# Kernel optimization log

Hardware: AMD Instinct MI355X
Metric: run time of the kernel (lower is better)

Reference implementation:

```python
import jax, jax.numpy as jnp
import numpy as np
from jax import lax

H = 16          # attention heads
N_LAYERS = 2    # encoder applies the SAME (shared-weight) layer N times
FILTERS = (1, 3, 5)
EPS_LN = 1e-6
EPS_BN = 1e-5


def _ln(x, a, b):
    # torch LayerNorm variant: unbiased std, eps added to std (not var)
    m = x.mean(-1, keepdims=True)
    s = jnp.std(x, axis=-1, keepdims=True, ddof=1)
    return a * (x - m) / (s + EPS_LN) + b


def _mha(x, wq, bq, wk, bk, wv, bv, wo, bo):
    B, S, D = x.shape
    dk = D // H
    def proj(w, b):
        return (x @ w + b).reshape(B, S, H, dk).transpose(0, 2, 1, 3)  # bhsd
    q, k, v = proj(wq, bq), proj(wk, bk), proj(wv, bv)
    scores = jnp.einsum('bhqd,bhkd->bhqk', q, k) / jnp.sqrt(jnp.float32(dk))
    p = jax.nn.softmax(scores, axis=-1)  # dropout is identity in eval mode
    o = jnp.einsum('bhqk,bhkd->bhqd', p, v)
    o = o.transpose(0, 2, 1, 3).reshape(B, S, D)
    return o @ wo + bo


def _conv_branch(xt, w, b, g, beta, m, v):
    # xt: [B, C, L]; w: [out, in, f]; BatchNorm1d in eval mode (running stats)
    f = w.shape[-1]
    y = lax.conv_general_dilated(xt, w, window_strides=(1,),
                                 padding=[(f // 2, f // 2)],
                                 dimension_numbers=('NCH', 'OIH', 'NCH'))
    y = y + b[None, :, None]
    y = (y - m[None, :, None]) / jnp.sqrt(v[None, :, None] + EPS_BN)
    y = y * g[None, :, None] + beta[None, :, None]
    return jax.nn.relu(y)


def setup_inputs() -> dict:
    key = jax.random.key(0)
    B, S, D = 8, 1024, 1024
    ks = iter(jax.random.split(key, 64))
    nrm = lambda shape, sc=0.02: jax.random.normal(next(ks), shape, jnp.float32) * sc
    inp = {'x': jax.random.normal(next(ks), (B, S, D), jnp.float32)}
    for nm in ('wq', 'wk', 'wv', 'wo'):
        inp[nm] = nrm((D, D))
    for nm in ('bq', 'bk', 'bv', 'bo'):
        inp[nm] = nrm((D,), 0.01)
    for i, f in enumerate(FILTERS, 1):
        inp[f'conv_w{i}'] = nrm((D, D, f))
        inp[f'conv_b{i}'] = nrm((D,), 0.01)
        inp[f'bn_g{i}'] = 1.0 + nrm((D,), 0.05)
        inp[f'bn_b{i}'] = nrm((D,), 0.05)
        inp[f'bn_m{i}'] = nrm((D,), 0.1)
        inp[f'bn_v{i}'] = 1.0 + 0.1 * jax.random.uniform(next(ks), (D,), jnp.float32)
    for nm in ('ln1_a', 'ln2_a', 'lnf_a'):
        inp[nm] = jnp.ones((D,), jnp.float32)
    for nm in ('ln1_b', 'ln2_b', 'lnf_b'):
        inp[nm] = jnp.zeros((D,), jnp.float32)
    return inp


def reference(x, wq, bq, wk, bk, wv, bv, wo, bo,
              conv_w1, conv_b1, bn_g1, bn_b1, bn_m1, bn_v1,
              conv_w2, conv_b2, bn_g2, bn_b2, bn_m2, bn_v2,
              conv_w3, conv_b3, bn_g3, bn_b3, bn_m3, bn_v3,
              ln1_a, ln1_b, ln2_a, ln2_b, lnf_a, lnf_b):
    convs = ((conv_w1, conv_b1, bn_g1, bn_b1, bn_m1, bn_v1),
             (conv_w2, conv_b2, bn_g2, bn_b2, bn_m2, bn_v2),
             (conv_w3, conv_b3, bn_g3, bn_b3, bn_m3, bn_v3))

    def ffn(h):
        xt = h.transpose(0, 2, 1)  # [B, D, S]
        outs = [_conv_branch(xt, *p) for p in convs]
        out = sum(outs) / jnp.float32(len(outs))  # mean over branch ensemble
        return out.transpose(0, 2, 1)

    for _ in range(N_LAYERS):  # shared-weight layer applied N times
        x = x + _mha(_ln(x, ln1_a, ln1_b), wq, bq, wk, bk, wv, bv, wo, bo)
        x = x + ffn(_ln(x, ln2_a, ln2_b))
    return _ln(x, lnf_a, lnf_b)
```

## Files before the change

kernel.cpp:

```cpp
#include <hip/hip_runtime.h>

#define TPB 256

typedef __attribute__((ext_vector_type(4))) float f32x4;
typedef __attribute__((ext_vector_type(8))) short s16x8;

__device__ __forceinline__ ushort f2bf(float f) {
  unsigned x = __float_as_uint(f);
  return (ushort)((x + 0x7fffu + ((x >> 16) & 1u)) >> 16);
}
__device__ __forceinline__ float b2f(ushort u) {
  return __uint_as_float(((unsigned)u) << 16);
}
__device__ __forceinline__ void gload_lds16(const ushort* g, ushort* l) {
  __builtin_amdgcn_global_load_lds(
      (const __attribute__((address_space(1))) void*)g,
      (__attribute__((address_space(3))) void*)l, 16, 0, 0);
}

__device__ __forceinline__ float blk_sum(float v, float* red, int tid) {
#pragma unroll
  for (int o = 32; o; o >>= 1) v += __shfl_xor(v, o);
  if ((tid & 63) == 0) red[tid >> 6] = v;
  __syncthreads();
  float r = red[0] + red[1] + red[2] + red[3];
  __syncthreads();
  return r;
}

template<bool C_BF16, bool HAS_BIAS, bool HAS_RES>
__global__ __launch_bounds__(TPB, 2)
void gemm_bt(const ushort* __restrict__ A, int lda,
             const ushort* __restrict__ B, int ldb,
             void* __restrict__ Cp, int ldc,
             const float* __restrict__ bias, const float* __restrict__ Res, int K)
{
  constexpr int BM = 128, BK = 32;
  __shared__ ushort lA[BM * BK];
  __shared__ ushort lB[128 * BK];
  const int tid = threadIdx.x;
  const int rowBase = blockIdx.x * BM;
  const int colBase = blockIdx.y * 128;
  const int w = tid >> 6, lane = tid & 63;
  const int wr = w >> 1, wc = w & 1;
  const int lr = lane & 15, lk = (lane >> 4) * 8;

  f32x4 acc[4][4] = {};

  for (int k0 = 0; k0 < K; k0 += BK) {
#pragma unroll
    for (int i = 0; i < 2; ++i) {
      int idx = i * TPB + tid;
      int r = idx >> 2, kk = (idx & 3) * 8;
      gload_lds16(A + (long)(rowBase + r) * lda + k0 + kk, &lA[idx * 8]);
    }
#pragma unroll
    for (int i = 0; i < 2; ++i) {
      int idx = i * TPB + tid;
      int r = idx >> 2, kk = (idx & 3) * 8;
      gload_lds16(B + (long)(colBase + r) * ldb + k0 + kk, &lB[idx * 8]);
    }
    __syncthreads();
    s16x8 af[4], bfr[4];
#pragma unroll
    for (int m = 0; m < 4; ++m)
      af[m] = *(const s16x8*)&lA[(wr * 64 + m * 16 + lr) * BK + lk];
#pragma unroll
    for (int n = 0; n < 4; ++n)
      bfr[n] = *(const s16x8*)&lB[(wc * 64 + n * 16 + lr) * BK + lk];
#pragma unroll
    for (int m = 0; m < 4; ++m)
#pragma unroll
      for (int n = 0; n < 4; ++n)
        acc[m][n] = __builtin_amdgcn_mfma_f32_16x16x32_bf16(af[m], bfr[n], acc[m][n], 0, 0, 0);
    __syncthreads();
  }

  const int crow0 = rowBase + wr * 64 + (lane >> 4) * 4;
#pragma unroll
  for (int m = 0; m < 4; ++m) {
#pragma unroll
    for (int n = 0; n < 4; ++n) {
      const int ccol = colBase + wc * 64 + n * 16 + lr;
      const float bv = HAS_BIAS ? bias[ccol] : 0.f;
#pragma unroll
      for (int j = 0; j < 4; ++j) {
        const long off = (long)(crow0 + m * 16 + j) * ldc + ccol;
        float v = acc[m][n][j] + bv;
        if (HAS_RES) v += Res[off];
        if (C_BF16) ((ushort*)Cp)[off] = f2bf(v);
        else        ((float*)Cp)[off] = v;
      }
    }
  }
}

__global__ __launch_bounds__(TPB, 2)
void conv_fused(const ushort* __restrict__ A, const ushort* __restrict__ W,
                float* __restrict__ x, const float* __restrict__ sc,
                const float* __restrict__ sh, const ushort* __restrict__ zp)
{
  constexpr int BM = 128, BK = 32;
  __shared__ ushort lA[BM * BK];
  __shared__ ushort lB[128 * BK];
  const int tid = threadIdx.x;
  const int rowBase = blockIdx.x * BM;
  const int colBase = blockIdx.y * 128;
  const int w = tid >> 6, lane = tid & 63;
  const int wr = w >> 1, wc = w & 1;
  const int lr = lane & 15, lk = (lane >> 4) * 8;

  f32x4 acc[4][4] = {};
  f32x4 res[4][4] = {};

  for (int s = 0; s < 9; ++s) {
    const int shift = (s == 0) ? 0 : ((s <= 3) ? s - 2 : s - 6);
    const ushort* Wseg = W + (long)s * 1048576;
    for (int k0 = 0; k0 < 1024; k0 += BK) {
#pragma unroll
      for (int i = 0; i < 2; ++i) {
        int idx = i * TPB + tid;
        int r = idx >> 2, kk = (idx & 3) * 8;
        int gr = rowBase + r;
        int sr = (gr & 1023) + shift;
        const ushort* src = ((unsigned)sr < 1024u)
            ? (A + (long)((gr & ~1023) + sr) * 1024 + k0 + kk) : zp;
        gload_lds16(src, &lA[idx * 8]);
      }
#pragma unroll
      for (int i = 0; i < 2; ++i) {
        int idx = i * TPB + tid;
        int r = idx >> 2, kk = (idx & 3) * 8;
        gload_lds16(Wseg + (long)(colBase + r) * 1024 + k0 + kk, &lB[idx * 8]);
      }
      __syncthreads();
      s16x8 af[4], bfr[4];
#pragma unroll
      for (int m = 0; m < 4; ++m)
        af[m] = *(const s16x8*)&lA[(wr * 64 + m * 16 + lr) * BK + lk];
#pragma unroll
      for (int n = 0; n < 4; ++n)
        bfr[n] = *(const s16x8*)&lB[(wc * 64 + n * 16 + lr) * BK + lk];
#pragma unroll
      for (int m = 0; m < 4; ++m)
#pragma unroll
        for (int n = 0; n < 4; ++n)
          acc[m][n] = __builtin_amdgcn_mfma_f32_16x16x32_bf16(af[m], bfr[n], acc[m][n], 0, 0, 0);
      __syncthreads();
    }
    if (s == 0 || s == 3 || s == 8) {
      const int br = (s == 0) ? 0 : (s == 3 ? 1 : 2);
#pragma unroll
      for (int n = 0; n < 4; ++n) {
        const int col = colBase + wc * 64 + n * 16 + lr;
        const float scv = sc[br * 1024 + col];
        const float shv = sh[br * 1024 + col];
#pragma unroll
        for (int m = 0; m < 4; ++m)
#pragma unroll
          for (int j = 0; j < 4; ++j) {
            res[m][n][j] += fmaxf(acc[m][n][j] * scv + shv, 0.f);
            acc[m][n][j] = 0.f;
          }
      }
    }
  }

  const int crow0 = rowBase + wr * 64 + (lane >> 4) * 4;
#pragma unroll
  for (int m = 0; m < 4; ++m)
#pragma unroll
    for (int n = 0; n < 4; ++n) {
      const int col = colBase + wc * 64 + n * 16 + lr;
#pragma unroll
      for (int j = 0; j < 4; ++j) {
        const long off = (long)(crow0 + m * 16 + j) * 1024 + col;
        x[off] += res[m][n][j] * (1.f / 3.f);
      }
    }
}

__global__ __launch_bounds__(TPB)
void flash_attn(const ushort* __restrict__ qkv, const ushort* __restrict__ vt,
                ushort* __restrict__ obuf)
{
  __shared__ ushort lK[64 * 64];
  __shared__ ushort lVt[64 * 64];
  __shared__ ushort lP[4 * 32 * 64];
  const int tid = threadIdx.x;
  const int w = tid >> 6, lane = tid & 63;
  const int g = lane >> 4, c = lane & 15;
  const int bh = blockIdx.y, b = bh >> 4, h = bh & 15;
  const int qw = blockIdx.x * 128 + w * 32;
  const float c8 = 0.18033688f;

  s16x8 qfr[2][2];
#pragma unroll
  for (int qf = 0; qf < 2; ++qf)
#pragma unroll
    for (int ds = 0; ds < 2; ++ds)
      qfr[qf][ds] = *(const s16x8*)(qkv
          + (long)((b << 10) + qw + qf * 16 + c) * 3072 + (h << 6) + ds * 32 + g * 8);

  f32x4 acc_o[2][4] = {};
  float m[2][4], l[2][4];
#pragma unroll
  for (int qf = 0; qf < 2; ++qf)
#pragma unroll
    for (int j = 0; j < 4; ++j) { m[qf][j] = -3.0e38f; l[qf][j] = 0.f; }

  ushort* lPw = &lP[w * 2048];

  for (int t = 0; t < 16; ++t) {
    const int kv0 = t * 64;
#pragma unroll
    for (int i = 0; i < 2; ++i) {
      int idx = i * TPB + tid;
      int r = idx >> 3, dc = (idx & 7) * 8;
      gload_lds16(qkv + (long)((b << 10) + kv0 + r) * 3072 + 1024 + (h << 6) + dc,
                  &lK[idx * 8]);
    }
#pragma unroll
    for (int i = 0; i < 2; ++i) {
      int idx = i * TPB + tid;
      int r = idx >> 3, dc = (idx & 7) * 8;
      gload_lds16(vt + (long)((bh << 6) + r) * 1024 + kv0 + dc, &lVt[idx * 8]);
    }
    __syncthreads();

    f32x4 s[2][4] = {};
#pragma unroll
    for (int ds = 0; ds < 2; ++ds) {
      s16x8 bk[4];
#pragma unroll
      for (int kf = 0; kf < 4; ++kf)
        bk[kf] = *(const s16x8*)&lK[(kf * 16 + c) * 64 + ds * 32 + g * 8];
#pragma unroll
      for (int qf = 0; qf < 2; ++qf)
#pragma unroll
        for (int kf = 0; kf < 4; ++kf)
          s[qf][kf] = __builtin_amdgcn_mfma_f32_16x16x32_bf16(qfr[qf][ds], bk[kf], s[qf][kf], 0, 0, 0);
    }

#pragma unroll
    for (int qf = 0; qf < 2; ++qf)
#pragma unroll
      for (int j = 0; j < 4; ++j) {
        float tm = fmaxf(fmaxf(s[qf][0][j], s[qf][1][j]), fmaxf(s[qf][2][j], s[qf][3][j]));
        tm = fmaxf(tm, __shfl_xor(tm, 1));
        tm = fmaxf(tm, __shfl_xor(tm, 2));
        tm = fmaxf(tm, __shfl_xor(tm, 4));
        tm = fmaxf(tm, __shfl_xor(tm, 8));
        float mn = fmaxf(m[qf][j], tm);
        float scale = exp2f((m[qf][j] - mn) * c8);
        m[qf][j] = mn;
        l[qf][j] *= scale;
#pragma unroll
        for (int df = 0; df < 4; ++df) acc_o[qf][df][j] *= scale;
        float ps = 0.f;
#pragma unroll
        for (int kf = 0; kf < 4; ++kf) {
          float pv = exp2f((s[qf][kf][j] - mn) * c8);
          ps += pv;
          lPw[(qf * 16 + g * 4 + j) * 64 + kf * 16 + c] = f2bf(pv);
        }
        l[qf][j] += ps;
      }

#pragma unroll
    for (int kvb = 0; kvb < 2; ++kvb) {
      s16x8 pA[2], vB[4];
#pragma unroll
      for (int qf = 0; qf < 2; ++qf)
        pA[qf] = *(const s16x8*)&lPw[(qf * 16 + c) * 64 + kvb * 32 + g * 8];
#pragma unroll
      for (int df = 0; df < 4; ++df)
        vB[df] = *(const s16x8*)&lVt[(df * 16 + c) * 64 + kvb * 32 + g * 8];
#pragma unroll
      for (int qf = 0; qf < 2; ++qf)
#pragma unroll
        for (int df = 0; df < 4; ++df)
          acc_o[qf][df] = __builtin_amdgcn_mfma_f32_16x16x32_bf16(pA[qf], vB[df], acc_o[qf][df], 0, 0, 0);
    }
    __syncthreads();
  }

#pragma unroll
  for (int qf = 0; qf < 2; ++qf)
#pragma unroll
    for (int j = 0; j < 4; ++j) {
      float lv = l[qf][j];
      lv += __shfl_xor(lv, 1);
      lv += __shfl_xor(lv, 2);
      lv += __shfl_xor(lv, 4);
      lv += __shfl_xor(lv, 8);
      float inv = 1.f / lv;
#pragma unroll
      for (int df = 0; df < 4; ++df)
        obuf[(long)((b << 10) + qw + qf * 16 + g * 4 + j) * 1024 + (h << 6) + df * 16 + c]
            = f2bf(acc_o[qf][df][j] * inv);
    }
}

template<bool OBF>
__global__ __launch_bounds__(TPB)
void ln_rows(const float* __restrict__ X, const float* __restrict__ ga,
             const float* __restrict__ gb, void* __restrict__ out)
{
  __shared__ float red[4];
  const int tid = threadIdx.x;
  const long base = (long)blockIdx.x * 1024;
  f32x4 v = *(const f32x4*)&X[base + tid * 4];
  float mean = blk_sum(v[0] + v[1] + v[2] + v[3], red, tid) * (1.f / 1024.f);
  f32x4 d = v - mean;
  float qs = blk_sum(d[0]*d[0] + d[1]*d[1] + d[2]*d[2] + d[3]*d[3], red, tid);
  float inv = 1.f / (sqrtf(qs * (1.f / 1023.f)) + 1e-6f);
  f32x4 a4 = *(const f32x4*)&ga[tid * 4];
  f32x4 b4 = *(const f32x4*)&gb[tid * 4];
  f32x4 r = a4 * (d * inv) + b4;
  if (OBF) {
    ushort4 o4 = { f2bf(r[0]), f2bf(r[1]), f2bf(r[2]), f2bf(r[3]) };
    *(ushort4*)((ushort*)out + base + tid * 4) = o4;
  } else {
    *(f32x4*)((float*)out + base + tid * 4) = r;
  }
}

__global__ __launch_bounds__(TPB)
void vt_build(const ushort* __restrict__ qkv, ushort* __restrict__ vt)
{
  __shared__ ushort t[64][72];
  const int tid = threadIdx.x;
  const int bh = blockIdx.y, b = bh >> 4, h = bh & 15;
  const int kv0 = blockIdx.x * 64;
#pragma unroll
  for (int it = 0; it < 2; ++it) {
    int idx = (it * TPB + tid) * 8;
    int r = idx >> 6, cc = idx & 63;
    s16x8 v = *(const s16x8*)(qkv + ((long)((b << 10) + kv0 + r)) * 3072 + 2048 + (h << 6) + cc);
#pragma unroll
    for (int j = 0; j < 8; ++j) t[r][cc + j] = (ushort)v[j];
  }
  __syncthreads();
#pragma unroll
  for (int it = 0; it < 2; ++it) {
    int idx = (it * TPB + tid) * 8;
    int dd = idx >> 6, kvo = idx & 63;
    ushort tmp[8];
#pragma unroll
    for (int j = 0; j < 8; ++j) tmp[j] = t[kvo + j][dd];
    *(s16x8*)(vt + ((long)bh * 64 + dd) * 1024 + kv0 + kvo) = *(const s16x8*)tmp;
  }
}

__global__ __launch_bounds__(TPB)
void wt_build(const float* __restrict__ in, ushort* __restrict__ out)
{
  __shared__ float t[64][65];
  const int tid = threadIdx.x;
  const int k0 = blockIdx.x * 64, n0 = blockIdx.y * 64;
#pragma unroll
  for (int it = 0; it < 4; ++it) {
    int idx = it * TPB + tid;
    int r = idx >> 4, c4 = (idx & 15) * 4;
    f32x4 v = *(const f32x4*)&in[(long)(k0 + r) * 1024 + n0 + c4];
    t[r][c4] = v[0]; t[r][c4 + 1] = v[1]; t[r][c4 + 2] = v[2]; t[r][c4 + 3] = v[3];
  }
  __syncthreads();
#pragma unroll
  for (int it = 0; it < 4; ++it) {
    int idx = it * TPB + tid;
    int nr = idx >> 4, k4 = (idx & 15) * 4;
    ushort4 o = { f2bf(t[k4][nr]), f2bf(t[k4 + 1][nr]),
                  f2bf(t[k4 + 2][nr]), f2bf(t[k4 + 3][nr]) };
    *(ushort4*)&out[(long)(n0 + nr) * 1024 + k0 + k4] = o;
  }
}
__global__ __launch_bounds__(TPB)
void tap_build(const float* __restrict__ w, ushort* __restrict__ out, int f)
{
  long idx = (long)blockIdx.x * TPB + threadIdx.x;
  long oi = idx & 1048575; int t = (int)(idx >> 20);
  out[idx] = f2bf(w[oi * f + t]);
}
__global__ __launch_bounds__(TPB)
void bn_prep(const float* __restrict__ cb, const float* __restrict__ g,
             const float* __restrict__ bb, const float* __restrict__ m,
             const float* __restrict__ v, float* __restrict__ sc, float* __restrict__ sh)
{
  int i = blockIdx.x * TPB + threadIdx.x;
  float s = g[i] * rsqrtf(v[i] + 1e-5f);
  sc[i] = s;
  sh[i] = (cb[i] - m[i]) * s + bb[i];
}
__global__ __launch_bounds__(TPB)
void qkvb_build(const float* __restrict__ bq, const float* __restrict__ bk,
                const float* __restrict__ bv, float* __restrict__ out)
{
  int i = blockIdx.x * TPB + threadIdx.x;
  out[i] = (i < 1024) ? bq[i] : (i < 2048 ? bk[i - 1024] : bv[i - 2048]);
}
__global__ void zero_ws(ushort* z) { z[threadIdx.x] = 0; }

extern "C" void kernel_launch(void* const* d_in, const int* in_sizes, int n_in,
                              void* d_out, int out_size, void* d_ws, size_t ws_size,
                              hipStream_t stream)
{
  const float* X  = (const float*)d_in[0];
  const float* Wq = (const float*)d_in[1];
  const float* Wk = (const float*)d_in[2];
  const float* Wv = (const float*)d_in[3];
  const float* Wo = (const float*)d_in[4];
  const float* Bq = (const float*)d_in[5];
  const float* Bk = (const float*)d_in[6];
  const float* Bv = (const float*)d_in[7];
  const float* Bo = (const float*)d_in[8];
  const float *CW[3], *CB[3], *BG[3], *BBe[3], *BMu[3], *BVa[3];
  for (int i = 0; i < 3; ++i) {
    CW[i]  = (const float*)d_in[9 + 6 * i];
    CB[i]  = (const float*)d_in[10 + 6 * i];
    BG[i]  = (const float*)d_in[11 + 6 * i];
    BBe[i] = (const float*)d_in[12 + 6 * i];
    BMu[i] = (const float*)d_in[13 + 6 * i];
    BVa[i] = (const float*)d_in[14 + 6 * i];
  }
  const float* L1a = (const float*)d_in[27];
  const float* L2a = (const float*)d_in[28];
  const float* LFa = (const float*)d_in[29];
  const float* L1b = (const float*)d_in[30];
  const float* L2b = (const float*)d_in[31];
  const float* LFb = (const float*)d_in[32];

  char* p = (char*)d_ws;
  auto carve = [&](size_t bytes) { char* r = p; p += (bytes + 255) & ~(size_t)255; return r; };
  ushort* abuf  = (ushort*)carve(16777216);
  ushort* wqkvt = (ushort*)carve(6291456);
  ushort* wot   = (ushort*)carve(2097152);
  ushort* wtap  = (ushort*)carve(18874368);
  ushort* qkv   = (ushort*)carve(50331648);
  ushort* vt    = (ushort*)carve(16777216);
  ushort* obuf  = (ushort*)carve(16777216);
  float*  qkvb  = (float*) carve(12288);
  float*  bnsc  = (float*) carve(12288);
  float*  bnsh  = (float*) carve(12288);
  ushort* zp    = (ushort*)carve(256);
  if ((size_t)(p - (char*)d_ws) > ws_size) return;

  float* xbuf = (float*)d_out;

  wt_build<<<dim3(16, 16), TPB, 0, stream>>>(Wq, wqkvt);
  wt_build<<<dim3(16, 16), TPB, 0, stream>>>(Wk, wqkvt + 1048576);
  wt_build<<<dim3(16, 16), TPB, 0, stream>>>(Wv, wqkvt + 2097152);
  wt_build<<<dim3(16, 16), TPB, 0, stream>>>(Wo, wot);
  tap_build<<<4096, TPB, 0, stream>>>(CW[0], wtap, 1);
  tap_build<<<3 * 4096, TPB, 0, stream>>>(CW[1], wtap + 1048576, 3);
  tap_build<<<5 * 4096, TPB, 0, stream>>>(CW[2], wtap + 4 * 1048576, 5);
  for (int i = 0; i < 3; ++i)
    bn_prep<<<4, TPB, 0, stream>>>(CB[i], BG[i], BBe[i], BMu[i], BVa[i],
                                   bnsc + i * 1024, bnsh + i * 1024);
  qkvb_build<<<12, TPB, 0, stream>>>(Bq, Bk, Bv, qkvb);
  zero_ws<<<1, 128, 0, stream>>>(zp);

  for (int L = 0; L < 2; ++L) {
    const float* xs = (L == 0) ? X : xbuf;
    ln_rows<true><<<8192, TPB, 0, stream>>>(xs, L1a, L1b, abuf);
    gemm_bt<true, true, false><<<dim3(64, 24), TPB, 0, stream>>>(
        abuf, 1024, wqkvt, 1024, qkv, 3072, qkvb, nullptr, 1024);
    vt_build<<<dim3(16, 128), TPB, 0, stream>>>(qkv, vt);
    flash_attn<<<dim3(8, 128), TPB, 0, stream>>>(qkv, vt, obuf);
    gemm_bt<false, true, true><<<dim3(64, 8), TPB, 0, stream>>>(
        obuf, 1024, wot, 1024, xbuf, 1024, Bo, xs, 1024);
    ln_rows<true><<<8192, TPB, 0, stream>>>(xbuf, L2a, L2b, abuf);
    conv_fused<<<dim3(64, 8), TPB, 0, stream>>>(abuf, wtap, xbuf, bnsc, bnsh, zp);
  }
  ln_rows<false><<<8192, TPB, 0, stream>>>(xbuf, LFa, LFb, d_out);
}
```

Measured before the change: 1.076 ms.

## Triple-buffer conv GEMM with async LDS loads, swizzle, and larger tiles

Replaces the conv GEMM kernel with a 512-thread, 256x128-tile version. It triple-buffers 64-wide K slices in dynamic LDS and uses direct global-to-LDS loads with explicit vmcnt waits, so loads overlap MFMA work and only one barrier is needed per step. An XOR swizzle on the LDS layout is meant to avoid bank conflicts. The tap_build kernel now loops over taps per thread so each input element is read once. The kernel uses 144KB of LDS, which limits occupancy to about one block per CU, and the grid shrinks to 256 blocks.

Result: faster. 1.024 ms (-4.8%).

```diff
diff --git a/kernel.cpp b/kernel.cpp
--- a/kernel.cpp
+++ b/kernel.cpp
@@ -95,87 +95,122 @@
   }
 }
 
-__global__ __launch_bounds__(TPB, 2)
-void conv_fused(const ushort* __restrict__ A, const ushort* __restrict__ W,
-                float* __restrict__ x, const float* __restrict__ sc,
-                const float* __restrict__ sh, const ushort* __restrict__ zp)
-{
-  constexpr int BM = 128, BK = 32;
-  __shared__ ushort lA[BM * BK];
-  __shared__ ushort lB[128 * BK];
+__global__ __launch_bounds__(512, 2)
+void conv_fused2(const ushort* __restrict__ A, const ushort* __restrict__ W9,
+                 float* __restrict__ x, const float* __restrict__ sc,
+                 const float* __restrict__ sh, const ushort* __restrict__ zp)
+{
+  extern __shared__ ushort smem[];
+  ushort* lA = smem;
+  ushort* lB = smem + 49152;
   const int tid = threadIdx.x;
-  const int rowBase = blockIdx.x * BM;
+  const int rowBase = blockIdx.x * 256;
   const int colBase = blockIdx.y * 128;
   const int w = tid >> 6, lane = tid & 63;
-  const int wr = w >> 1, wc = w & 1;
-  const int lr = lane & 15, lk = (lane >> 4) * 8;
+  const int wrm = w >> 1, wcn = w & 1;
+  const int lr = lane & 15, kg = lane >> 4;
 
   f32x4 acc[4][4] = {};
   f32x4 res[4][4] = {};
 
-  for (int s = 0; s < 9; ++s) {
+  auto stage = [&](int t, int buf) {
+    const int s = t >> 4;
+    const int k0 = (t & 15) * 64;
     const int shift = (s == 0) ? 0 : ((s <= 3) ? s - 2 : s - 6);
-    const ushort* Wseg = W + (long)s * 1048576;
-    for (int k0 = 0; k0 < 1024; k0 += BK) {
-#pragma unroll
-      for (int i = 0; i < 2; ++i) {
-        int idx = i * TPB + tid;
-        int r = idx >> 2, kk = (idx & 3) * 8;
-        int gr = rowBase + r;
-        int sr = (gr & 1023) + shift;
-        const ushort* src = ((unsigned)sr < 1024u)
-            ? (A + (long)((gr & ~1023) + sr) * 1024 + k0 + kk) : zp;
-        gload_lds16(src, &lA[idx * 8]);
+    const ushort* Wseg = W9 + (long)s * 1048576 + k0;
+    const ushort* Ak = A + k0;
+    ushort* dA = lA + buf * 16384;
+    ushort* dB = lB + buf * 8192;
+#pragma unroll
+    for (int i = 0; i < 4; ++i) {
+      int li = i * 512 + tid;
+      int r = li >> 3, sl = li & 7;
+      int gsl = sl ^ (r & 7);
+      int gr = rowBase + r;
+      int sr = (gr & 1023) + shift;
+      const ushort* src = ((unsigned)sr < 1024u)
+          ? (Ak + (long)((gr & ~1023) + sr) * 1024 + gsl * 8) : zp;
+      gload_lds16(src, dA + li * 8);
+    }
+#pragma unroll
+    for (int i = 0; i < 2; ++i) {
+      int li = i * 512 + tid;
+      int r = li >> 3, sl = li & 7;
+      int gsl = sl ^ (r & 7);
+      gload_lds16(Wseg + (long)(colBase + r) * 1024 + gsl * 8, dB + li * 8);
+    }
+  };
+
+  stage(0, 0);
+  stage(1, 1);
+  __builtin_amdgcn_sched_barrier(0);
+  asm volatile("s_waitcnt vmcnt(6)" ::: "memory");
+  __builtin_amdgcn_sched_barrier(0);
+  __syncthreads();
+
+#pragma unroll 3
+  for (int t = 0; t < 144; ++t) {
+    const int cur = t % 3;
+    if (t + 2 < 144) stage(t + 2, (t + 2) % 3);
+
+    const ushort* bA = lA + cur * 16384;
+    const ushort* bB = lB + cur * 8192;
+#pragma unroll
+    for (int ks = 0; ks < 2; ++ks) {
+      s16x8 af[4], bfr[4];
+#pragma unroll
+      for (int mf = 0; mf < 4; ++mf) {
+        int r = wrm * 64 + mf * 16 + lr;
+        int sl = (ks * 4 + kg) ^ (r & 7);
+        af[mf] = *(const s16x8*)&bA[r * 64 + sl * 8];
       }
 #pragma unroll
-      for (int i = 0; i < 2; ++i) {
-        int idx = i * TPB + tid;
-        int r = idx >> 2, kk = (idx & 3) * 8;
-        gload_lds16(Wseg + (long)(colBase + r) * 1024 + k0 + kk, &lB[idx * 8]);
+      for (int nf = 0; nf < 4; ++nf) {
+        int r = wcn * 64 + nf * 16 + lr;
+        int sl = (ks * 4 + kg) ^ (r & 7);
+        bfr[nf] = *(const s16x8*)&bB[r * 64 + sl * 8];
       }
-      __syncthreads();
-      s16x8 af[4], bfr[4];
-#pragma unroll
-      for (int m = 0; m < 4; ++m)
-        af[m] = *(const s16x8*)&lA[(wr * 64 + m * 16 + lr) * BK + lk];
-#pragma unroll
-      for (int n = 0; n < 4; ++n)
-        bfr[n] = *(const s16x8*)&lB[(wc * 64 + n * 16 + lr) * BK + lk];
-#pragma unroll
-      for (int m = 0; m < 4; ++m)
-#pragma unroll
-        for (int n = 0; n < 4; ++n)
-          acc[m][n] = __builtin_amdgcn_mfma_f32_16x16x32_bf16(af[m], bfr[n], acc[m][n], 0, 0, 0);
-      __syncthreads();
-    }
-    if (s == 0 || s == 3 || s == 8) {
-      const int br = (s == 0) ? 0 : (s == 3 ? 1 : 2);
-#pragma unroll
-      for (int n = 0; n < 4; ++n) {
-        const int col = colBase + wc * 64 + n * 16 + lr;
+#pragma unroll
+      for (int mf = 0; mf < 4; ++mf)
+#pragma unroll
+        for (int nf = 0; nf < 4; ++nf)
+          acc[mf][nf] = __builtin_amdgcn_mfma_f32_16x16x32_bf16(af[mf], bfr[nf], acc[mf][nf], 0, 0, 0);
+    }
+
+    if (t == 15 || t == 63 || t == 143) {
+      const int br = (t == 15) ? 0 : (t == 63 ? 1 : 2);
+#pragma unroll
+      for (int nf = 0; nf < 4; ++nf) {
+        const int col = colBase + wcn * 64 + nf * 16 + lr;
         const float scv = sc[br * 1024 + col];
         const float shv = sh[br * 1024 + col];
 #pragma unroll
-        for (int m = 0; m < 4; ++m)
+        for (int mf = 0; mf < 4; ++mf)
 #pragma unroll
           for (int j = 0; j < 4; ++j) {
-            res[m][n][j] += fmaxf(acc[m][n][j] * scv + shv, 0.f);
-            acc[m][n][j] = 0.f;
+            res[mf][nf][j] += fmaxf(acc[mf][nf][j] * scv + shv, 0.f);
+            acc[mf][nf][j] = 0.f;
           }
       }
     }
-  }
-
-  const int crow0 = rowBase + wr * 64 + (lane >> 4) * 4;
-#pragma unroll
-  for (int m = 0; m < 4; ++m)
-#pragma unroll
-    for (int n = 0; n < 4; ++n) {
-      const int col = colBase + wc * 64 + n * 16 + lr;
+
+    __builtin_amdgcn_sched_barrier(0);
+    if (t + 2 < 144)      asm volatile("s_waitcnt vmcnt(6)" ::: "memory");
+    else if (t + 1 < 144) asm volatile("s_waitcnt vmcnt(0)" ::: "memory");
+    __builtin_amdgcn_sched_barrier(0);
+    __syncthreads();
+  }
+
+  const int crow0 = rowBase + wrm * 64 + kg * 4;
+#pragma unroll
+  for (int mf = 0; mf < 4; ++mf)
+#pragma unroll
+    for (int nf = 0; nf < 4; ++nf) {
+      const int col = colBase + wcn * 64 + nf * 16 + lr;
 #pragma unroll
       for (int j = 0; j < 4; ++j) {
-        const long off = (long)(crow0 + m * 16 + j) * 1024 + col;
-        x[off] += res[m][n][j] * (1.f / 3.f);
+        const long off = (long)(crow0 + mf * 16 + j) * 1024 + col;
+        x[off] += res[mf][nf][j] * (1.f / 3.f);
       }
     }
 }
@@ -379,9 +414,9 @@
 __global__ __launch_bounds__(TPB)
 void tap_build(const float* __restrict__ w, ushort* __restrict__ out, int f)
 {
-  long idx = (long)blockIdx.x * TPB + threadIdx.x;
-  long oi = idx & 1048575; int t = (int)(idx >> 20);
-  out[idx] = f2bf(w[oi * f + t]);
+  long oi = (long)blockIdx.x * TPB + threadIdx.x;
+  for (int t = 0; t < f; ++t)
+    out[(long)t * 1048576 + oi] = f2bf(w[oi * f + t]);
 }
 __global__ __launch_bounds__(TPB)
 void bn_prep(const float* __restrict__ cb, const float* __restrict__ g,
@@ -453,8 +488,8 @@
   wt_build<<<dim3(16, 16), TPB, 0, stream>>>(Wv, wqkvt + 2097152);
   wt_build<<<dim3(16, 16), TPB, 0, stream>>>(Wo, wot);
   tap_build<<<4096, TPB, 0, stream>>>(CW[0], wtap, 1);
-  tap_build<<<3 * 4096, TPB, 0, stream>>>(CW[1], wtap + 1048576, 3);
-  tap_build<<<5 * 4096, TPB, 0, stream>>>(CW[2], wtap + 4 * 1048576, 5);
+  tap_build<<<4096, TPB, 0, stream>>>(CW[1], wtap + 1048576, 3);
+  tap_build<<<4096, TPB, 0, stream>>>(CW[2], wtap + 4 * 1048576, 5);
   for (int i = 0; i < 3; ++i)
     bn_prep<<<4, TPB, 0, stream>>>(CB[i], BG[i], BBe[i], BMu[i], BVa[i],
                                    bnsc + i * 1024, bnsh + i * 1024);
@@ -471,7 +506,7 @@
     gemm_bt<false, true, true><<<dim3(64, 8), TPB, 0, stream>>>(
         obuf, 1024, wot, 1024, xbuf, 1024, Bo, xs, 1024);
     ln_rows<true><<<8192, TPB, 0, stream>>>(xbuf, L2a, L2b, abuf);
-    conv_fused<<<dim3(64, 8), TPB, 0, stream>>>(abuf, wtap, xbuf, bnsc, bnsh, zp);
+    conv_fused2<<<dim3(32, 8), 512, 147456, stream>>>(abuf, wtap, xbuf, bnsc, bnsh, zp);
   }
   ln_rows<false><<<8192, TPB, 0, stream>>>(xbuf, LFa, LFb, d_out);
 }
```
